# Optimization experiments

Hardware: AMD Instinct MI355X
Metric: run time of the kernel (lower is better)

## Reference

```python
import jax, jax.numpy as jnp
import numpy as np

CH = 512
GROUPS = 8
EPS = 1e-5


def setup_inputs() -> dict:
    key = jax.random.key(0)
    ks = jax.random.split(key, 5)
    B, C, H, W = 16, CH, 32, 32
    x = jax.random.normal(ks[0], (B, C, H, W), dtype=jnp.float32)
    # GroupNorm affine params
    norm_w = jnp.ones((C,), dtype=jnp.float32)
    norm_b = jnp.zeros((C,), dtype=jnp.float32)
    # 1x1 conv == linear over channels; store weights as [out, in]
    qkv_w = jax.random.normal(ks[1], (3 * C, C), dtype=jnp.float32) * (C ** -0.5)
    qkv_b = jnp.zeros((3 * C,), dtype=jnp.float32)
    proj_w = jax.random.normal(ks[2], (C, C), dtype=jnp.float32) * (C ** -0.5)
    proj_b = jnp.zeros((C,), dtype=jnp.float32)
    return {"x": x, "norm_w": norm_w, "norm_b": norm_b,
            "qkv_w": qkv_w, "qkv_b": qkv_b,
            "proj_w": proj_w, "proj_b": proj_b}


def _group_norm(x, w, b):
    B, C, H, W = x.shape
    g = GROUPS
    xg = x.reshape(B, g, C // g, H * W)
    mean = xg.mean(axis=(2, 3), keepdims=True)
    var = xg.var(axis=(2, 3), keepdims=True)
    xn = (xg - mean) * jax.lax.rsqrt(var + EPS)
    xn = xn.reshape(B, C, H, W)
    return xn * w[None, :, None, None] + b[None, :, None, None]


def reference(x, norm_w, norm_b, qkv_w, qkv_b, proj_w, proj_b):
    B, C, H, W = x.shape
    h = _group_norm(x, norm_w, norm_b)  # [B,C,H,W]
    hs = h.reshape(B, C, H * W)  # spatial tokens along last axis
    # 1x1 conv QKV: [3C,C] @ [B,C,N] -> [B,3C,N]
    qkv = jnp.einsum('oc,bcn->bon', qkv_w, hs) + qkv_b[None, :, None]
    q, k, v = jnp.split(qkv, 3, axis=1)  # each [B,C,N]
    scale = C ** (-0.5)
    attn = jnp.einsum('bci,bcj->bij', q, k) * scale  # [B,N,N]
    attn = jax.nn.softmax(attn, axis=-1)
    out = jnp.einsum('bij,bcj->bci', attn, v)  # [B,C,N]
    out = jnp.einsum('oc,bcn->bon', proj_w, out) + proj_b[None, :, None]
    return x + out.reshape(B, C, H, W)
```

## Files before the change

### kernel.cpp

```cpp
#include <hip/hip_runtime.h>
#include <math.h>

#define Bn   16
#define Cn   512
#define Nn   1024
#define Gn   8
#define CPG  64
#define EPSf 1e-5f

typedef short           bf16x8 __attribute__((ext_vector_type(8)));
typedef float           f32x4  __attribute__((ext_vector_type(4)));
typedef unsigned short  u16;
typedef unsigned short  u16x4  __attribute__((ext_vector_type(4)));
typedef unsigned short  u16x8  __attribute__((ext_vector_type(8)));

#define TS 136

__device__ __forceinline__ u16 f2b(float f) {
  union { float f; unsigned u; } c; c.f = f;
  unsigned r = (c.u + 0x7FFFu + ((c.u >> 16) & 1u)) >> 16;
  return (u16)r;
}

__device__ __forceinline__ void g2l16(const void* g, void* l) {
  __builtin_amdgcn_global_load_lds(
      (const __attribute__((address_space(1))) unsigned int*)g,
      (__attribute__((address_space(3))) unsigned int*)l, 16, 0, 0);
}

__device__ __forceinline__ void barrier_asm() {
  asm volatile("s_barrier" ::: "memory");
}

__device__ __forceinline__ void gemm_core(u16* As, u16* Bs,
    const u16* __restrict__ A, size_t sA,
    const u16* __restrict__ B, size_t sB, int K, f32x4 acc[4][4]) {
  const int t = threadIdx.x;
  const int w = t >> 6, l = t & 63, quad = l >> 4, lr = l & 15;
  const int wm = (w >> 1) * 64, wn = (w & 1) * 64;

  const int ra = w * 16 + (l >> 2);
  const int p  = l & 3;
  const int q  = p ^ ((ra >> 1) & 3);
  const u16* gA0 = A + (size_t)ra * sA + q * 8;
  const u16* gA1 = A + (size_t)(ra + 64) * sA + q * 8;
  const u16* gB0 = B + (size_t)ra * sB + q * 8;
  const u16* gB1 = B + (size_t)(ra + 64) * sB + q * 8;
  u16* lA0 = As + ra * 32 + p * 8;
  u16* lA1 = As + (ra + 64) * 32 + p * 8;
  u16* lB0 = Bs + ra * 32 + p * 8;
  u16* lB1 = Bs + (ra + 64) * 32 + p * 8;

  for (int k0 = 0; k0 < K; k0 += 32) {
    __syncthreads();
    g2l16(gA0 + k0, lA0);
    g2l16(gA1 + k0, lA1);
    g2l16(gB0 + k0, lB0);
    g2l16(gB1 + k0, lB1);
    __syncthreads();
    bf16x8 af[4], bfr[4];
    #pragma unroll
    for (int fm = 0; fm < 4; fm++) {
      int r = wm + fm * 16 + lr;
      af[fm] = *(const bf16x8*)&As[r * 32 + ((quad ^ ((r >> 1) & 3)) << 3)];
    }
    #pragma unroll
    for (int fn = 0; fn < 4; fn++) {
      int r = wn + fn * 16 + lr;
      bfr[fn] = *(const bf16x8*)&Bs[r * 32 + ((quad ^ ((r >> 1) & 3)) << 3)];
    }
    #pragma unroll
    for (int fm = 0; fm < 4; fm++)
      #pragma unroll
      for (int fn = 0; fn < 4; fn++)
        acc[fm][fn] = __builtin_amdgcn_mfma_f32_16x16x32_bf16(
            af[fm], bfr[fn], acc[fm][fn], 0, 0, 0);
  }
}

#define GEMM_PRE()                                              \
  const int t = threadIdx.x;                                    \
  const int w = t >> 6, l = t & 63, quad = l >> 4, lr = l & 15; \
  const int wm = (w >> 1) * 64, wn = (w & 1) * 64;              \
  (void)w; (void)wm; (void)wn; (void)l;                         \
  f32x4 acc[4][4];                                              \
  { f32x4 z = {0.f, 0.f, 0.f, 0.f};                             \
    for (int i_ = 0; i_ < 4; i_++)                              \
      for (int j_ = 0; j_ < 4; j_++) acc[i_][j_] = z; }

#define SLOT 12288

__device__ __forceinline__ void core256(const u16* __restrict__ A, size_t sA,
    const u16* __restrict__ B, size_t sB, int K, u16* SH, f32x4 acc[8][4],
    int wm, int wn, int quad, int lr) {
  const int t = threadIdx.x, wv = t >> 6, l = t & 63;
  const int srow = l >> 2;
  const int sch  = ((l & 3) ^ ((l >> 3) & 3)) * 8;

  const u16* gA[4]; int lA[4];
  const u16* gB[2]; int lB[2];
  #pragma unroll
  for (int c = 0; c < 4; c++) {
    gA[c] = A + (size_t)(wv * 64 + c * 16 + srow) * sA + sch;
    lA[c] = wv * 2048 + c * 512 + l * 8;
  }
  #pragma unroll
  for (int c = 0; c < 2; c++) {
    gB[c] = B + (size_t)(wv * 32 + c * 16 + srow) * sB + sch;
    lB[c] = 8192 + wv * 1024 + c * 512 + l * 8;
  }

  u16 *sc = SH, *sn = SH + SLOT, *sf = SH + 2 * SLOT;
  #pragma unroll
  for (int c = 0; c < 4; c++) g2l16(gA[c], sc + lA[c]);
  #pragma unroll
  for (int c = 0; c < 2; c++) g2l16(gB[c], sc + lB[c]);

  const int rch = (quad ^ ((lr >> 1) & 3)) * 8;
  int aoff[8], boff[4];
  #pragma unroll
  for (int fm = 0; fm < 8; fm++) aoff[fm] = (wm + fm * 16 + lr) * 32 + rch;
  #pragma unroll
  for (int fn = 0; fn < 4; fn++) boff[fn] = 8192 + (wn + fn * 16 + lr) * 32 + rch;

  const int nt = K >> 5;
  for (int tt = 0; tt < nt; tt++) {
    if (tt + 1 < nt) {
      const int k0 = (tt + 1) * 32;
      #pragma unroll
      for (int c = 0; c < 4; c++) g2l16(gA[c] + k0, sn + lA[c]);
      #pragma unroll
      for (int c = 0; c < 2; c++) g2l16(gB[c] + k0, sn + lB[c]);
      asm volatile("s_waitcnt vmcnt(6)" ::: "memory");
    } else {
      asm volatile("s_waitcnt vmcnt(0)" ::: "memory");
    }
    barrier_asm();
    bf16x8 af[8], bfr[4];
    #pragma unroll
    for (int fm = 0; fm < 8; fm++) af[fm] = *(const bf16x8*)&sc[aoff[fm]];
    #pragma unroll
    for (int fn = 0; fn < 4; fn++) bfr[fn] = *(const bf16x8*)&sc[boff[fn]];
    __builtin_amdgcn_s_setprio(1);
    #pragma unroll
    for (int fm = 0; fm < 8; fm++)
      #pragma unroll
      for (int fn = 0; fn < 4; fn++)
        acc[fm][fn] = __builtin_amdgcn_mfma_f32_16x16x32_bf16(
            af[fm], bfr[fn], acc[fm][fn], 0, 0, 0);
    __builtin_amdgcn_s_setprio(0);
    u16* tmp = sc; sc = sn; sn = sf; sf = tmp;
  }
}

#define CORE256_PRE()                                             \
  const int t = threadIdx.x;                                      \
  const int w = t >> 6, l = t & 63, quad = l >> 4, lr = l & 15;   \
  const int wm = (w >> 1) * 128, wn = (w & 1) * 64;               \
  (void)l;                                                        \
  f32x4 acc[8][4];                                                \
  { f32x4 z = {0.f, 0.f, 0.f, 0.f};                               \
    _Pragma("unroll")                                             \
    for (int i_ = 0; i_ < 8; i_++)                                \
      _Pragma("unroll")                                           \
      for (int j_ = 0; j_ < 4; j_++) acc[i_][j_] = z; }

__global__ __launch_bounds__(256) void prep_k(const float* __restrict__ qkv_w,
    const float* __restrict__ proj_w, const float* __restrict__ qkv_b,
    const float* __restrict__ x, u16* __restrict__ wqk16,
    u16* __restrict__ wvT16, u16* __restrict__ pw16,
    float* __restrict__ bias2, float* __restrict__ stats) {
  __shared__ u16 T[64][68];
  __shared__ float redf[8];
  int bid = blockIdx.x, t = threadIdx.x;
  if (bid < 512) {
    int i = bid * 256 + t;
    float4 v = ((const float4*)qkv_w)[i];
    u16x4 o;
    o.x = f2b(v.x); o.y = f2b(v.y); o.z = f2b(v.z); o.w = f2b(v.w);
    ((u16x4*)wqk16)[i] = o;
  } else if (bid < 576) {
    int tile = bid - 512, tx = tile & 7, ty = tile >> 3;
    int row = t >> 4, col4 = t & 15;
    #pragma unroll
    for (int it = 0; it < 4; it++) {
      int cc = row + it * 16;
      float4 v = *(const float4*)&qkv_w[(size_t)(1024 + ty * 64 + cc) * 512 + tx * 64 + col4 * 4];
      u16x4 o;
      o.x = f2b(v.x); o.y = f2b(v.y); o.z = f2b(v.z); o.w = f2b(v.w);
      *(u16x4*)&T[cc][col4 * 4] = o;
    }
    __syncthreads();
    #pragma unroll
    for (int it = 0; it < 2; it++) {
      int ch = t + it * 256;
      int d = ch >> 3, c8 = (ch & 7) * 8;
      u16x8 o;
      #pragma unroll
      for (int j = 0; j < 8; j++) o[j] = T[c8 + j][d];
      *(u16x8*)&wvT16[(size_t)(tx * 64 + d) * 512 + ty * 64 + c8] = o;
    }
  } else if (bid < 578) {
    int m = (bid - 576) * 256 + t;
    float s = 0.f;
    for (int c = 0; c < 512; c++)
      s += proj_w[(size_t)m * 512 + c] * qkv_b[1024 + c];
    bias2[m] = s;
  } else if (bid < 1090) {
    int idx = bid - 578, bg = idx >> 2, part = idx & 3;
    const float4* xp = (const float4*)x + (size_t)bg * 16384 + part * 4096;
    float s = 0.f, ss = 0.f;
    for (int i = t; i < 4096; i += 256) {
      float4 v = xp[i];
      s  += v.x + v.y + v.z + v.w;
      ss += v.x * v.x + v.y * v.y + v.z * v.z + v.w * v.w;
    }
    #pragma unroll
    for (int off = 32; off > 0; off >>= 1) {
      s  += __shfl_down(s, off);
      ss += __shfl_down(ss, off);
    }
    int lane = t & 63, wid = t >> 6;
    if (lane == 0) { redf[wid] = s; redf[4 + wid] = ss; }
    __syncthreads();
    if (t == 0) {
      atomicAdd(&stats[bg],       redf[0] + redf[1] + redf[2] + redf[3]);
      atomicAdd(&stats[128 + bg], redf[4] + redf[5] + redf[6] + redf[7]);
    }
  } else {
    int i = (bid - 1090) * 256 + t;
    float4 v = ((const float4*)proj_w)[i];
    u16x4 o;
    o.x = f2b(v.x); o.y = f2b(v.y); o.z = f2b(v.z); o.w = f2b(v.w);
    ((u16x4*)pw16)[i] = o;
  }
}

__global__ __launch_bounds__(256) void gnw2_k(const float* __restrict__ x,
    const float* __restrict__ stats, const float* __restrict__ nw,
    const float* __restrict__ nb, const u16* __restrict__ pw16,
    const u16* __restrict__ wvT16, u16* __restrict__ W2, u16* __restrict__ hT) {
  __shared__ u16 AsBs[8192];
  int bid = blockIdx.x;
  if (bid < 16) {
    int m0 = (bid >> 2) * 128, d0 = (bid & 3) * 128;
    GEMM_PRE();
    gemm_core(AsBs, AsBs + 4096, pw16 + (size_t)m0 * 512, 512,
              wvT16 + (size_t)d0 * 512, 512, 512, acc);
    #pragma unroll
    for (int fm = 0; fm < 4; fm++) {
      int m = m0 + wm + fm * 16 + quad * 4;
      #pragma unroll
      for (int fn = 0; fn < 4; fn++) {
        int d = d0 + wn + fn * 16 + lr;
        f32x4 a = acc[fm][fn];
        W2[(size_t)(m    ) * 512 + d] = f2b(a[0]);
        W2[(size_t)(m + 1) * 512 + d] = f2b(a[1]);
        W2[(size_t)(m + 2) * 512 + d] = f2b(a[2]);
        W2[(size_t)(m + 3) * 512 + d] = f2b(a[3]);
      }
    }
    return;
  }
  int u = bid - 16;
  int b = u >> 7, rem = u & 127, c0 = (rem >> 4) * 64, n0 = (rem & 15) * 64;
  u16 (*T)[68] = (u16(*)[68])AsBs;
  int t = threadIdx.x;
  int row = t >> 4, col4 = t & 15;
  const float inv = 1.0f / 65536.0f;
  #pragma unroll
  for (int it = 0; it < 4; it++) {
    int cc = row + it * 16;
    int c  = c0 + cc;
    int bg = b * Gn + (c >> 6);
    float mean = stats[bg] * inv;
    float var  = stats[128 + bg] * inv - mean * mean;
    float rstd = rsqrtf(var + EPSf);
    float a  = nw[c] * rstd;
    float bb = nb[c] - mean * a;
    float4 xv = *(const float4*)&x[((size_t)(b * Cn + c)) * Nn + n0 + col4 * 4];
    u16x4 o;
    o.x = f2b(xv.x * a + bb); o.y = f2b(xv.y * a + bb);
    o.z = f2b(xv.z * a + bb); o.w = f2b(xv.w * a + bb);
    *(u16x4*)&T[cc][col4 * 4] = o;
  }
  __syncthreads();
  #pragma unroll
  for (int it = 0; it < 2; it++) {
    int ch = t + it * 256;
    int n  = ch >> 3, c8 = (ch & 7) * 8;
    u16x8 o;
    #pragma unroll
    for (int j = 0; j < 8; j++) o[j] = T[c8 + j][n];
    *(u16x8*)&hT[((size_t)(b * Nn + n0 + n)) * 512 + c0 + c8] = o;
  }
}

__global__ __launch_bounds__(256, 2) void qkvp_k(const u16* __restrict__ wqk16,
    const u16* __restrict__ W2, const u16* __restrict__ hT,
    const float* __restrict__ qkv_b, u16* __restrict__ qkT,
    u16* __restrict__ VP) {
  __shared__ __align__(16) u16 SH[3 * SLOT];
  int u = blockIdx.x;
  CORE256_PRE();

  if (u < 512) {
    int b = u >> 5, rem = u & 31, m0 = (rem >> 3) * 256, n0 = (rem & 7) * 128;
    core256(wqk16 + (size_t)m0 * 512, 512,
            hT + (size_t)(b * Nn + n0) * 512, 512, 512, SH, acc, wm, wn, quad, lr);
    float4 bss[8];
    #pragma unroll
    for (int fm = 0; fm < 8; fm++)
      bss[fm] = *(const float4*)&qkv_b[m0 + wm + fm * 16 + quad * 4];
    u16* T = SH;
    const int hsel = wn >> 6;
    #pragma unroll
    for (int h = 0; h < 2; h++) {
      barrier_asm();
      if (hsel == h) {
        #pragma unroll
        for (int fm = 0; fm < 8; fm++) {
          int mc = wm + fm * 16 + quad * 4;
          #pragma unroll
          for (int fn = 0; fn < 4; fn++) {
            int nl = fn * 16 + lr;
            f32x4 a = acc[fm][fn];
            u16x4 pk;
            pk.x = f2b(a[0] + bss[fm].x); pk.y = f2b(a[1] + bss[fm].y);
            pk.z = f2b(a[2] + bss[fm].z); pk.w = f2b(a[3] + bss[fm].w);
            *(u16x4*)&T[nl * 264 + mc] = pk;
          }
        }
      }
      barrier_asm();
      #pragma unroll
      for (int kk = 0; kk < 8; kk++) {
        int idx = t + 256 * kk, row = idx >> 5, grp = idx & 31;
        u16x8 v = *(u16x8*)&T[row * 264 + grp * 8];
        *(u16x8*)&qkT[((size_t)(b * Nn + n0 + h * 64 + row)) * 1024 + m0 + grp * 8] = v;
      }
    }
  } else {
    int u2 = u - 512;
    int b = u2 >> 4, rem = u2 & 15, m0 = (rem >> 3) * 256, j0 = (rem & 7) * 128;
    core256(W2 + (size_t)m0 * 512, 512,
            hT + (size_t)(b * Nn + j0) * 512, 512, 512, SH, acc, wm, wn, quad, lr);
    u16* T = SH;
    const int hsel = wm >> 7;
    #pragma unroll
    for (int h = 0; h < 2; h++) {
      barrier_asm();
      if (hsel == h) {
        #pragma unroll
        for (int fm = 0; fm < 8; fm++) {
          int ml = fm * 16 + quad * 4;
          #pragma unroll
          for (int fn = 0; fn < 4; fn++) {
            int jl = wn + fn * 16 + lr;
            f32x4 a = acc[fm][fn];
            T[(ml    ) * TS + jl] = f2b(a[0]);
            T[(ml + 1) * TS + jl] = f2b(a[1]);
            T[(ml + 2) * TS + jl] = f2b(a[2]);
            T[(ml + 3) * TS + jl] = f2b(a[3]);
          }
        }
      }
      barrier_asm();
      #pragma unroll
      for (int kk = 0; kk < 8; kk++) {
        int idx = t + 256 * kk, row = idx >> 4, grp = idx & 15;
        u16x8 v = *(u16x8*)&T[row * TS + grp * 8];
        *(u16x8*)&VP[((size_t)(b * 512 + m0 + h * 128 + row)) * 1024 + j0 + grp * 8] = v;
      }
    }
  }
}

__global__ __launch_bounds__(256, 2) void qkexp_k(const u16* __restrict__ qkT,
    u16* __restrict__ Pm, float* __restrict__ rpart) {
  __shared__ __align__(16) u16 SH[3 * SLOT];
  __shared__ float psum[256];
  int u = blockIdx.x;
  int b = u >> 5, rem = u & 31, i0 = (rem >> 3) * 256, j0 = (rem & 7) * 128;
  const u16* base = qkT + (size_t)b * Nn * 1024;
  CORE256_PRE();
  core256(base + (size_t)i0 * 1024, 1024,
          base + (size_t)j0 * 1024 + 512, 1024, 512, SH, acc, wm, wn, quad, lr);
  psum[t] = 0.f;
  const float scale = 0.04419417382415922f;
  u16* T = SH;
  const int hsel = wm >> 7;
  #pragma unroll
  for (int h = 0; h < 2; h++) {
    barrier_asm();
    if (hsel == h) {
      #pragma unroll
      for (int fm = 0; fm < 8; fm++) {
        int il = fm * 16 + quad * 4;
        float rs0 = 0.f, rs1 = 0.f, rs2 = 0.f, rs3 = 0.f;
        #pragma unroll
        for (int fn = 0; fn < 4; fn++) {
          int jl = wn + fn * 16 + lr;
          f32x4 a = acc[fm][fn];
          float e0 = __expf(a[0] * scale);
          float e1 = __expf(a[1] * scale);
          float e2 = __expf(a[2] * scale);
          float e3 = __expf(a[3] * scale);
          rs0 += e0; rs1 += e1; rs2 += e2; rs3 += e3;
          T[(il    ) * TS + jl] = f2b(e0);
          T[(il + 1) * TS + jl] = f2b(e1);
          T[(il + 2) * TS + jl] = f2b(e2);
          T[(il + 3) * TS + jl] = f2b(e3);
        }
        #pragma unroll
        for (int mask = 1; mask < 16; mask <<= 1) {
          rs0 += __shfl_xor(rs0, mask);
          rs1 += __shfl_xor(rs1, mask);
          rs2 += __shfl_xor(rs2, mask);
          rs3 += __shfl_xor(rs3, mask);
        }
        if (lr == 0) {
          int ri = h * 128 + il;
          atomicAdd(&psum[ri],     rs0);
          atomicAdd(&psum[ri + 1], rs1);
          atomicAdd(&psum[ri + 2], rs2);
          atomicAdd(&psum[ri + 3], rs3);
        }
      }
    }
    barrier_asm();
    #pragma unroll
    for (int kk = 0; kk < 8; kk++) {
      int idx = t + 256 * kk, row = idx >> 4, grp = idx & 15;
      u16x8 v = *(u16x8*)&T[row * TS + grp * 8];
      *(u16x8*)&Pm[((size_t)(b * Nn + i0 + h * 128 + row)) * 1024 + j0 + grp * 8] = v;
    }
  }
  __syncthreads();
  rpart[((size_t)(b * 8) + (rem & 7)) * 1024 + i0 + t] = psum[t];
}

__global__ __launch_bounds__(256, 2) void pvout_k(const u16* __restrict__ VP,
    const u16* __restrict__ Pm, const float* __restrict__ rpart,
    const float* __restrict__ bias2, const float* __restrict__ proj_b,
    const float* __restrict__ x, float* __restrict__ out) {
  __shared__ __align__(16) u16 SH[3 * SLOT];
  __shared__ float rinv[128];
  int bid = blockIdx.x;
  int b = bid >> 4, rem = bid & 15, m0 = (rem >> 3) * 256, i0 = (rem & 7) * 128;
  if (threadIdx.x < 128) {
    float s = 0.f;
    #pragma unroll
    for (int jb = 0; jb < 8; jb++)
      s += rpart[((size_t)(b * 8 + jb)) * 1024 + i0 + threadIdx.x];
    rinv[threadIdx.x] = 1.0f / s;
  }
  CORE256_PRE();
  core256(VP + ((size_t)(b * 512 + m0)) * 1024, 1024,
          Pm + ((size_t)(b * Nn + i0)) * 1024, 1024, 1024, SH, acc, wm, wn, quad, lr);
  __syncthreads();
  #pragma unroll
  for (int fm = 0; fm < 8; fm++) {
    int m = m0 + wm + fm * 16 + quad * 4;
    float c0 = bias2[m    ] + proj_b[m    ];
    float c1 = bias2[m + 1] + proj_b[m + 1];
    float c2 = bias2[m + 2] + proj_b[m + 2];
    float c3 = bias2[m + 3] + proj_b[m + 3];
    #pragma unroll
    for (int fn = 0; fn < 4; fn++) {
      int il = wn + fn * 16 + lr;
      int i  = i0 + il;
      float ri = rinv[il];
      f32x4 a = acc[fm][fn];
      size_t o0 = ((size_t)(b * Cn + m)) * Nn + i;
      out[o0                  ] = a[0] * ri + c0 + x[o0                  ];
      out[o0 + Nn             ] = a[1] * ri + c1 + x[o0 + Nn             ];
      out[o0 + 2 * Nn         ] = a[2] * ri + c2 + x[o0 + 2 * Nn         ];
      out[o0 + 3 * (size_t)Nn] = a[3] * ri + c3 + x[o0 + 3 * (size_t)Nn];
    }
  }
}

extern "C" void kernel_launch(void* const* d_in, const int* in_sizes, int n_in,
                              void* d_out, int out_size, void* d_ws, size_t ws_size,
                              hipStream_t stream) {
  const float* x      = (const float*)d_in[0];
  const float* norm_w = (const float*)d_in[1];
  const float* norm_b = (const float*)d_in[2];
  const float* qkv_w  = (const float*)d_in[3];
  const float* qkv_b  = (const float*)d_in[4];
  const float* proj_w = (const float*)d_in[5];
  const float* proj_b = (const float*)d_in[6];
  float* out = (float*)d_out;
  char* ws = (char*)d_ws;

  u16*   wqk16 = (u16*)(ws);
  u16*   wvT16 = (u16*)(ws + 1048576);
  u16*   pw16  = (u16*)(ws + 1572864);
  u16*   W2    = (u16*)(ws + 2097152);
  float* bias2 = (float*)(ws + 2621440);
  float* stats = (float*)(ws + 2623488);
  u16*   hT    = (u16*)(ws + 2624512);
  u16*   qkT   = (u16*)(ws + 19401728);
  u16*   VP    = (u16*)(ws + 52956160);
  u16*   Pm    = (u16*)(ws + 69733376);
  float* rpart = (float*)(ws + 103287808);

  hipMemsetAsync(stats, 0, 1024, stream);
  prep_k<<<1346, 256, 0, stream>>>(qkv_w, proj_w, qkv_b, x, wqk16, wvT16,
                                   pw16, bias2, stats);
  gnw2_k<<<2064, 256, 0, stream>>>(x, stats, norm_w, norm_b, pw16, wvT16,
                                   W2, hT);
  qkvp_k<<<768, 256, 0, stream>>>(wqk16, W2, hT, qkv_b, qkT, VP);
  qkexp_k<<<512, 256, 0, stream>>>(qkT, Pm, rpart);
  pvout_k<<<256, 256, 0, stream>>>(VP, Pm, rpart, bias2, proj_b, x, out);
}
```

Before: 228.1 us.

## Use 128x128 tiles with 4-stage pipeline and swizzled block order in pvout

```diff
diff --git a/kernel.cpp b/kernel.cpp
--- a/kernel.cpp
+++ b/kernel.cpp
@@ -164,6 +164,73 @@
     for (int i_ = 0; i_ < 8; i_++)                                \
       _Pragma("unroll")                                           \
       for (int j_ = 0; j_ < 4; j_++) acc[i_][j_] = z; }
+
+#define SLOT128 8192
+
+__device__ __forceinline__ void core128(const u16* __restrict__ A, size_t sA,
+    const u16* __restrict__ B, size_t sB, int K, u16* SH, f32x4 acc[4][4],
+    int wm, int wn, int quad, int lr) {
+  const int t = threadIdx.x;
+  const int w = t >> 6, l = t & 63;
+  const int ra = w * 16 + (l >> 2);
+  const int p  = l & 3;
+  const int q  = p ^ ((ra >> 1) & 3);
+  const u16* gA0 = A + (size_t)ra * sA + q * 8;
+  const u16* gA1 = A + (size_t)(ra + 64) * sA + q * 8;
+  const u16* gB0 = B + (size_t)ra * sB + q * 8;
+  const u16* gB1 = B + (size_t)(ra + 64) * sB + q * 8;
+  const int lA0 = ra * 32 + p * 8;
+  const int lA1 = (ra + 64) * 32 + p * 8;
+  const int lB0 = 4096 + ra * 32 + p * 8;
+  const int lB1 = 4096 + (ra + 64) * 32 + p * 8;
+
+  const int nt = K >> 5;
+  {
+    u16* s0 = SH;
+    g2l16(gA0, s0 + lA0); g2l16(gA1, s0 + lA1);
+    g2l16(gB0, s0 + lB0); g2l16(gB1, s0 + lB1);
+    if (nt > 1) {
+      u16* s1 = SH + SLOT128;
+      g2l16(gA0 + 32, s1 + lA0); g2l16(gA1 + 32, s1 + lA1);
+      g2l16(gB0 + 32, s1 + lB0); g2l16(gB1 + 32, s1 + lB1);
+    }
+  }
+  const int rch = (quad ^ ((lr >> 1) & 3)) * 8;
+  int aoff[4], boff[4];
+  #pragma unroll
+  for (int fm = 0; fm < 4; fm++) aoff[fm] = (wm + fm * 16 + lr) * 32 + rch;
+  #pragma unroll
+  for (int fn = 0; fn < 4; fn++) boff[fn] = 4096 + (wn + fn * 16 + lr) * 32 + rch;
+
+  for (int tt = 0; tt < nt; tt++) {
+    u16* sc = SH + (tt & 3) * SLOT128;
+    if (tt + 2 < nt) {
+      u16* sn = SH + ((tt + 2) & 3) * SLOT128;
+      const int k0 = (tt + 2) * 32;
+      g2l16(gA0 + k0, sn + lA0); g2l16(gA1 + k0, sn + lA1);
+      g2l16(gB0 + k0, sn + lB0); g2l16(gB1 + k0, sn + lB1);
+      asm volatile("s_waitcnt vmcnt(8)" ::: "memory");
+    } else if (tt + 1 < nt) {
+      asm volatile("s_waitcnt vmcnt(4)" ::: "memory");
+    } else {
+      asm volatile("s_waitcnt vmcnt(0)" ::: "memory");
+    }
+    barrier_asm();
+    bf16x8 af[4], bfr[4];
+    #pragma unroll
+    for (int fm = 0; fm < 4; fm++) af[fm] = *(const bf16x8*)&sc[aoff[fm]];
+    #pragma unroll
+    for (int fn = 0; fn < 4; fn++) bfr[fn] = *(const bf16x8*)&sc[boff[fn]];
+    __builtin_amdgcn_s_setprio(1);
+    #pragma unroll
+    for (int fm = 0; fm < 4; fm++)
+      #pragma unroll
+      for (int fn = 0; fn < 4; fn++)
+        acc[fm][fn] = __builtin_amdgcn_mfma_f32_16x16x32_bf16(
+            af[fm], bfr[fn], acc[fm][fn], 0, 0, 0);
+    __builtin_amdgcn_s_setprio(0);
+  }
+}
 
 __global__ __launch_bounds__(256) void prep_k(const float* __restrict__ qkv_w,
     const float* __restrict__ proj_w, const float* __restrict__ qkv_b,
@@ -444,10 +511,11 @@
     const u16* __restrict__ Pm, const float* __restrict__ rpart,
     const float* __restrict__ bias2, const float* __restrict__ proj_b,
     const float* __restrict__ x, float* __restrict__ out) {
-  __shared__ __align__(16) u16 SH[3 * SLOT];
+  __shared__ __align__(16) u16 SH[4 * SLOT128];
   __shared__ float rinv[128];
   int bid = blockIdx.x;
-  int b = bid >> 4, rem = bid & 15, m0 = (rem >> 3) * 256, i0 = (rem & 7) * 128;
+  int u = (bid & 7) * 64 + (bid >> 3);
+  int b = u >> 5, rem = u & 31, m0 = (rem >> 3) * 128, i0 = (rem & 7) * 128;
   if (threadIdx.x < 128) {
     float s = 0.f;
     #pragma unroll
@@ -455,12 +523,12 @@
       s += rpart[((size_t)(b * 8 + jb)) * 1024 + i0 + threadIdx.x];
     rinv[threadIdx.x] = 1.0f / s;
   }
-  CORE256_PRE();
-  core256(VP + ((size_t)(b * 512 + m0)) * 1024, 1024,
+  GEMM_PRE();
+  core128(VP + ((size_t)(b * 512 + m0)) * 1024, 1024,
           Pm + ((size_t)(b * Nn + i0)) * 1024, 1024, 1024, SH, acc, wm, wn, quad, lr);
   __syncthreads();
   #pragma unroll
-  for (int fm = 0; fm < 8; fm++) {
+  for (int fm = 0; fm < 4; fm++) {
     int m = m0 + wm + fm * 16 + quad * 4;
     float c0 = bias2[m    ] + proj_b[m    ];
     float c1 = bias2[m + 1] + proj_b[m + 1];
@@ -513,5 +581,5 @@
                                    W2, hT);
   qkvp_k<<<768, 256, 0, stream>>>(wqk16, W2, hT, qkv_b, qkT, VP);
   qkexp_k<<<512, 256, 0, stream>>>(qkT, Pm, rpart);
-  pvout_k<<<256, 256, 0, stream>>>(VP, Pm, rpart, bias2, proj_b, x, out);
-}
+  pvout_k<<<512, 256, 0, stream>>>(VP, Pm, rpart, bias2, proj_b, x, out);
+}
```

New measurement: 217.5 us. 4.7% less time.
